# Kernel tuning notes

Hardware: AMD Instinct MI355X
Metric: run time of the kernel (lower is better)

The kernel has to match this reference:

```python
import jax, jax.numpy as jnp
import numpy as np

B, C, H, W = 16, 64, 64, 64
K = 1024  # n_embedding


def setup_inputs() -> dict:
    key = jax.random.key(0)
    k1, k2 = jax.random.split(key)
    x = jax.random.normal(k1, (B, C, H, W), dtype=jnp.float32)
    embedding = jax.random.normal(k2, (K, C), dtype=jnp.float32)
    return {"x": x, "embedding": embedding}


def reference(x, embedding):
    b, c, h, w = x.shape
    # [B,C,H,W] -> [N, C] tokens
    xf = jnp.transpose(x, (0, 2, 3, 1)).reshape(-1, c)
    # squared Euclidean distances (argmin-equivalent to torch.cdist p=2)
    d2 = (jnp.sum(xf * xf, axis=1, keepdims=True)
          - 2.0 * xf @ embedding.T
          + jnp.sum(embedding * embedding, axis=1)[None, :])  # [N, K]
    idx = jnp.argmin(d2, axis=-1)  # [N]
    q = embedding[idx]             # gather: [N, C]
    commitment_loss = jnp.mean((jax.lax.stop_gradient(q) - xf) ** 2)
    codebook_loss = jnp.mean((q - jax.lax.stop_gradient(xf)) ** 2)
    # straight-through estimator
    out = xf + jax.lax.stop_gradient(q - xf)
    x_q = jnp.transpose(out.reshape(b, h, w, c), (0, 3, 1, 2))
    indices = idx.reshape(-1, h, w)
    return x_q, codebook_loss, commitment_loss, indices
```

## Files before the change

kernel.cpp:

```cpp
#include <hip/hip_runtime.h>

typedef short s16x8 __attribute__((ext_vector_type(8)));
typedef float f32x4 __attribute__((ext_vector_type(4)));

#define NTOK 65536
#define CCH 64
#define KCB 1024
#define HWSZ 4096
#define CHW 262144
#define NXQ 4194304
#define NMEAN 4194304.0
#define PLANE_BYTES 131072

static __device__ __forceinline__ unsigned short f2bf(float f) {
    unsigned int u = __float_as_uint(f);
    return (unsigned short)((u + 0x7FFFu + ((u >> 16) & 1u)) >> 16);
}
static __device__ __forceinline__ float bf2f(unsigned short b) {
    return __uint_as_float(((unsigned int)b) << 16);
}

__global__ void vq_prep(const float* __restrict__ E, float* __restrict__ e2,
                        s16x8* __restrict__ Bh, s16x8* __restrict__ Bm,
                        s16x8* __restrict__ Bl, double* __restrict__ loss_acc) {
    int gid = blockIdx.x * blockDim.x + threadIdx.x;
    if (gid == 0) *loss_acc = 0.0;
    {
        int nt = gid >> 7, rem = gid & 127;
        int ks = rem >> 6, l = rem & 63;
        int code = nt * 16 + (l & 15);
        int cb   = ks * 32 + ((l >> 4) << 3);
        const float* ep = E + code * CCH + cb;
        s16x8 vh, vm, vl;
#pragma unroll
        for (int j = 0; j < 8; ++j) {
            float v = -2.f * ep[j];
            unsigned short h  = f2bf(v);  float r1 = v  - bf2f(h);
            unsigned short md = f2bf(r1); float r2 = r1 - bf2f(md);
            unsigned short lo = f2bf(r2);
            vh[j] = (short)h; vm[j] = (short)md; vl[j] = (short)lo;
        }
        Bh[gid] = vh; Bm[gid] = vm; Bl[gid] = vl;
    }
    if (gid < KCB) {
        const float4* e4 = reinterpret_cast<const float4*>(E + gid * CCH);
        float s = 0.f;
#pragma unroll
        for (int i = 0; i < 16; ++i) {
            float4 v = e4[i];
            s = fmaf(v.x, v.x, s); s = fmaf(v.y, v.y, s);
            s = fmaf(v.z, v.z, s); s = fmaf(v.w, v.w, s);
        }
        e2[gid] = s;
    }
}

__global__ __launch_bounds__(512, 2) void vq_main(
    const float* __restrict__ x, const float* __restrict__ E,
    const s16x8* __restrict__ Bh, const s16x8* __restrict__ Bm,
    const s16x8* __restrict__ Bl, const float* __restrict__ e2,
    float* __restrict__ out, double* __restrict__ loss_acc)
{
    __shared__ __align__(16) short XH[64 * 64];
    __shared__ __align__(16) short XM[64 * 64];
    __shared__ __align__(16) short XL[64 * 64];
    __shared__ float XSQ[8][64];
    __shared__ float SB[8][64];
    __shared__ int   SI[8][64];

    const int t    = threadIdx.x;
    const int lane = t & 63;
    const int w    = t >> 6;
    const int n0   = blockIdx.x * 64;
    const int b    = n0 >> 12;
    const int hw0  = n0 & 4095;

    {
        const int tok = t & 63;
        const int cb  = t >> 6;
        const float* xp = x + b * CHW + hw0 + tok;
        float xs = 0.f;
        s16x8 ph, pm, pl;
#pragma unroll
        for (int j = 0; j < 8; ++j) {
            float v = xp[(cb * 8 + j) * HWSZ];
            xs = fmaf(v, v, xs);
            unsigned short h  = f2bf(v);  float r1 = v  - bf2f(h);
            unsigned short md = f2bf(r1); float r2 = r1 - bf2f(md);
            unsigned short lo = f2bf(r2);
            ph[j] = (short)h; pm[j] = (short)md; pl[j] = (short)lo;
        }
        XSQ[cb][tok] = xs;
        const int wofs = tok * 128 + ((cb * 16) ^ ((tok & 7) << 4));
        *reinterpret_cast<s16x8*>((char*)XH + wofs) = ph;
        *reinterpret_cast<s16x8*>((char*)XM + wofs) = pm;
        *reinterpret_cast<s16x8*>((char*)XL + wofs) = pl;
    }
    __syncthreads();

    const int g   = lane >> 4;
    const int c15 = lane & 15;

    s16x8 ah[4][2], am[4][2], al[4][2];
#pragma unroll
    for (int m = 0; m < 4; ++m) {
        const int row = m * 16 + c15;
        const int rb  = row * 128;
        const int swz = (row & 7) << 4;
#pragma unroll
        for (int ks = 0; ks < 2; ++ks) {
            int off = rb + ((ks * 64 + g * 16) ^ swz);
            ah[m][ks] = *reinterpret_cast<const s16x8*>((const char*)XH + off);
            am[m][ks] = *reinterpret_cast<const s16x8*>((const char*)XM + off);
            al[m][ks] = *reinterpret_cast<const s16x8*>((const char*)XL + off);
        }
    }

    float e2w[8];
#pragma unroll
    for (int i = 0; i < 8; ++i) e2w[i] = e2[w * 128 + i * 16 + c15];

    float best[4][4];
    int   bidx[4][4];
#pragma unroll
    for (int m = 0; m < 4; ++m)
#pragma unroll
        for (int r = 0; r < 4; ++r) { best[m][r] = 3.4e38f; bidx[m][r] = 0; }

#pragma unroll 1
    for (int ch = 0; ch < 4; ++ch) {
        s16x8 bh[2][2], bm[2][2], bl[2][2];
#pragma unroll
        for (int nt = 0; nt < 2; ++nt)
#pragma unroll
            for (int ks = 0; ks < 2; ++ks) {
                int idx = ((w * 8 + ch * 2 + nt) * 2 + ks) * 64 + lane;
                bh[nt][ks] = Bh[idx];
                bm[nt][ks] = Bm[idx];
                bl[nt][ks] = Bl[idx];
            }

        f32x4 acc[4][2];
#pragma unroll
        for (int m = 0; m < 4; ++m)
#pragma unroll
            for (int nt = 0; nt < 2; ++nt) {
                float s0 = e2w[ch * 2 + nt];
                acc[m][nt] = (f32x4){s0, s0, s0, s0};
            }

#pragma unroll
        for (int m = 0; m < 4; ++m)
#pragma unroll
            for (int nt = 0; nt < 2; ++nt)
#pragma unroll
                for (int ks = 0; ks < 2; ++ks) {
                    acc[m][nt] = __builtin_amdgcn_mfma_f32_16x16x32_bf16(ah[m][ks], bh[nt][ks], acc[m][nt], 0, 0, 0);
                    acc[m][nt] = __builtin_amdgcn_mfma_f32_16x16x32_bf16(ah[m][ks], bm[nt][ks], acc[m][nt], 0, 0, 0);
                    acc[m][nt] = __builtin_amdgcn_mfma_f32_16x16x32_bf16(am[m][ks], bh[nt][ks], acc[m][nt], 0, 0, 0);
                    acc[m][nt] = __builtin_amdgcn_mfma_f32_16x16x32_bf16(am[m][ks], bm[nt][ks], acc[m][nt], 0, 0, 0);
                    acc[m][nt] = __builtin_amdgcn_mfma_f32_16x16x32_bf16(ah[m][ks], bl[nt][ks], acc[m][nt], 0, 0, 0);
                    acc[m][nt] = __builtin_amdgcn_mfma_f32_16x16x32_bf16(al[m][ks], bh[nt][ks], acc[m][nt], 0, 0, 0);
                }

#pragma unroll
        for (int nt = 0; nt < 2; ++nt) {
            const int k = w * 128 + ch * 32 + nt * 16 + c15;
#pragma unroll
            for (int m = 0; m < 4; ++m)
#pragma unroll
                for (int r = 0; r < 4; ++r) {
                    float s = acc[m][nt][r];
                    if (s < best[m][r]) { best[m][r] = s; bidx[m][r] = k; }
                }
        }
    }

#pragma unroll
    for (int m = 0; m < 4; ++m)
#pragma unroll
        for (int r = 0; r < 4; ++r) {
            float v = best[m][r]; int k = bidx[m][r];
#pragma unroll
            for (int off = 1; off < 16; off <<= 1) {
                float ov = __shfl_xor(v, off, 64);
                int   ok = __shfl_xor(k, off, 64);
                if (ov < v || (ov == v && ok < k)) { v = ov; k = ok; }
            }
            if (c15 == 0) {
                int tk = m * 16 + g * 4 + r;
                SB[w][tk] = v; SI[w][tk] = k;
            }
        }
    __syncthreads();

    if (w == 0) {
        float bv = SB[0][lane]; int bi = SI[0][lane];
#pragma unroll
        for (int ww = 1; ww < 8; ++ww) {
            float v = SB[ww][lane];
            if (v < bv) { bv = v; bi = SI[ww][lane]; }
        }
        out[NXQ + 2 + n0 + lane] = (float)bi;

        float xsq = 0.f;
#pragma unroll
        for (int c = 0; c < 8; ++c) xsq += XSQ[c][lane];
        float lsum = bv + xsq;
#pragma unroll
        for (int off = 32; off > 0; off >>= 1)
            lsum += __shfl_xor(lsum, off, 64);
        if (lane == 0) atomicAdd(loss_acc, (double)lsum);

        const float4* eq = reinterpret_cast<const float4*>(E + bi * CCH);
        float* oq = out + b * CHW + hw0 + lane;
#pragma unroll 1
        for (int gq = 0; gq < 4; ++gq) {
            float4 q0 = eq[4 * gq + 0];
            float4 q1 = eq[4 * gq + 1];
            float4 q2 = eq[4 * gq + 2];
            float4 q3 = eq[4 * gq + 3];
            float* o = oq + (16 * gq) * HWSZ;
            o[0 * HWSZ] = q0.x; o[1 * HWSZ]  = q0.y; o[2 * HWSZ]  = q0.z; o[3 * HWSZ]  = q0.w;
            o[4 * HWSZ] = q1.x; o[5 * HWSZ]  = q1.y; o[6 * HWSZ]  = q1.z; o[7 * HWSZ]  = q1.w;
            o[8 * HWSZ] = q2.x; o[9 * HWSZ]  = q2.y; o[10 * HWSZ] = q2.z; o[11 * HWSZ] = q2.w;
            o[12 * HWSZ] = q3.x; o[13 * HWSZ] = q3.y; o[14 * HWSZ] = q3.z; o[15 * HWSZ] = q3.w;
        }
    }
}

__global__ void vq_final(const double* __restrict__ loss_acc,
                         float* __restrict__ out) {
    if (threadIdx.x == 0) {
        float m = (float)(*loss_acc / NMEAN);
        out[NXQ]     = m;
        out[NXQ + 1] = m;
    }
}

extern "C" void kernel_launch(void* const* d_in, const int* in_sizes, int n_in,
                              void* d_out, int out_size, void* d_ws, size_t ws_size,
                              hipStream_t stream) {
    const float* x = (const float*)d_in[0];
    const float* E = (const float*)d_in[1];
    float* out = (float*)d_out;
    double* loss_acc = (double*)d_ws;
    float*  e2 = (float*)((char*)d_ws + 64);
    s16x8*  Bh = (s16x8*)((char*)d_ws + 8192);
    s16x8*  Bm = (s16x8*)((char*)d_ws + 8192 + PLANE_BYTES);
    s16x8*  Bl = (s16x8*)((char*)d_ws + 8192 + 2 * PLANE_BYTES);

    vq_prep <<<32,   256, 0, stream>>>(E, e2, Bh, Bm, Bl, loss_acc);
    vq_main <<<1024, 512, 0, stream>>>(x, E, Bh, Bm, Bl, e2, out, loss_acc);
    vq_final<<<1,    64,  0, stream>>>(loss_acc, out);
}
```

Before: 145.9 us.

## Restructure VQ kernel: warps own token tiles, stream codebook through double-buffered LDS

New measurement: 128.3 us. 12.0% less time.

```diff
diff --git a/kernel.cpp b/kernel.cpp
--- a/kernel.cpp
+++ b/kernel.cpp
@@ -3,7 +3,6 @@
 typedef short s16x8 __attribute__((ext_vector_type(8)));
 typedef float f32x4 __attribute__((ext_vector_type(4)));
 
-#define NTOK 65536
 #define CCH 64
 #define KCB 1024
 #define HWSZ 4096
@@ -55,132 +54,107 @@
     }
 }
 
-__global__ __launch_bounds__(512, 2) void vq_main(
+__global__ __launch_bounds__(256, 2) void vq_main(
     const float* __restrict__ x, const float* __restrict__ E,
     const s16x8* __restrict__ Bh, const s16x8* __restrict__ Bm,
     const s16x8* __restrict__ Bl, const float* __restrict__ e2,
     float* __restrict__ out, double* __restrict__ loss_acc)
 {
-    __shared__ __align__(16) short XH[64 * 64];
-    __shared__ __align__(16) short XM[64 * 64];
-    __shared__ __align__(16) short XL[64 * 64];
-    __shared__ float XSQ[8][64];
-    __shared__ float SB[8][64];
-    __shared__ int   SI[8][64];
+    __shared__ s16x8 BB[2][768];
+    __shared__ float BVL[128];
+    __shared__ int   BIL[128];
+    __shared__ float XSL[128];
 
     const int t    = threadIdx.x;
     const int lane = t & 63;
     const int w    = t >> 6;
-    const int n0   = blockIdx.x * 64;
+    const int g    = lane >> 4;
+    const int c15  = lane & 15;
+    const int n0   = blockIdx.x * 128;
     const int b    = n0 >> 12;
     const int hw0  = n0 & 4095;
 
-    {
-        const int tok = t & 63;
-        const int cb  = t >> 6;
-        const float* xp = x + b * CHW + hw0 + tok;
+    s16x8 ah[2][2], am[2][2], al[2][2];
+#pragma unroll
+    for (int mt = 0; mt < 2; ++mt) {
+        const float* xp = x + b * CHW + hw0 + w * 32 + mt * 16 + c15;
         float xs = 0.f;
-        s16x8 ph, pm, pl;
-#pragma unroll
-        for (int j = 0; j < 8; ++j) {
-            float v = xp[(cb * 8 + j) * HWSZ];
-            xs = fmaf(v, v, xs);
-            unsigned short h  = f2bf(v);  float r1 = v  - bf2f(h);
-            unsigned short md = f2bf(r1); float r2 = r1 - bf2f(md);
-            unsigned short lo = f2bf(r2);
-            ph[j] = (short)h; pm[j] = (short)md; pl[j] = (short)lo;
-        }
-        XSQ[cb][tok] = xs;
-        const int wofs = tok * 128 + ((cb * 16) ^ ((tok & 7) << 4));
-        *reinterpret_cast<s16x8*>((char*)XH + wofs) = ph;
-        *reinterpret_cast<s16x8*>((char*)XM + wofs) = pm;
-        *reinterpret_cast<s16x8*>((char*)XL + wofs) = pl;
-    }
+#pragma unroll
+        for (int ks = 0; ks < 2; ++ks)
+#pragma unroll
+            for (int j = 0; j < 8; ++j) {
+                float v = xp[(ks * 32 + g * 8 + j) * HWSZ];
+                xs = fmaf(v, v, xs);
+                unsigned short h  = f2bf(v);  float r1 = v  - bf2f(h);
+                unsigned short md = f2bf(r1); float r2 = r1 - bf2f(md);
+                unsigned short lo = f2bf(r2);
+                ah[mt][ks][j] = (short)h; am[mt][ks][j] = (short)md; al[mt][ks][j] = (short)lo;
+            }
+        xs += __shfl_xor(xs, 16, 64);
+        xs += __shfl_xor(xs, 32, 64);
+        if (lane < 16) XSL[w * 32 + mt * 16 + lane] = xs;
+    }
+
+    BB[0][t] = Bh[t]; BB[0][256 + t] = Bm[t]; BB[0][512 + t] = Bl[t];
     __syncthreads();
 
-    const int g   = lane >> 4;
-    const int c15 = lane & 15;
-
-    s16x8 ah[4][2], am[4][2], al[4][2];
-#pragma unroll
-    for (int m = 0; m < 4; ++m) {
-        const int row = m * 16 + c15;
-        const int rb  = row * 128;
-        const int swz = (row & 7) << 4;
-#pragma unroll
-        for (int ks = 0; ks < 2; ++ks) {
-            int off = rb + ((ks * 64 + g * 16) ^ swz);
-            ah[m][ks] = *reinterpret_cast<const s16x8*>((const char*)XH + off);
-            am[m][ks] = *reinterpret_cast<const s16x8*>((const char*)XM + off);
-            al[m][ks] = *reinterpret_cast<const s16x8*>((const char*)XL + off);
-        }
-    }
-
-    float e2w[8];
-#pragma unroll
-    for (int i = 0; i < 8; ++i) e2w[i] = e2[w * 128 + i * 16 + c15];
-
-    float best[4][4];
-    int   bidx[4][4];
-#pragma unroll
-    for (int m = 0; m < 4; ++m)
-#pragma unroll
-        for (int r = 0; r < 4; ++r) { best[m][r] = 3.4e38f; bidx[m][r] = 0; }
-
+    float best[2][4]; int bidx[2][4];
+#pragma unroll
+    for (int mt = 0; mt < 2; ++mt)
+#pragma unroll
+        for (int r = 0; r < 4; ++r) { best[mt][r] = 3.4e38f; bidx[mt][r] = 0; }
+
+    int buf = 0;
 #pragma unroll 1
-    for (int ch = 0; ch < 4; ++ch) {
-        s16x8 bh[2][2], bm[2][2], bl[2][2];
-#pragma unroll
-        for (int nt = 0; nt < 2; ++nt)
+    for (int ch = 0; ch < 32; ++ch) {
+        s16x8 sH, sM, sL;
+        const int nb = (ch + 1) * 256 + t;
+        if (ch < 31) { sH = Bh[nb]; sM = Bm[nb]; sL = Bl[nb]; }
+
+#pragma unroll
+        for (int nt = 0; nt < 2; ++nt) {
+            const float s0 = e2[ch * 32 + nt * 16 + c15];
+            s16x8 bh[2], bm[2], bl[2];
 #pragma unroll
             for (int ks = 0; ks < 2; ++ks) {
-                int idx = ((w * 8 + ch * 2 + nt) * 2 + ks) * 64 + lane;
-                bh[nt][ks] = Bh[idx];
-                bm[nt][ks] = Bm[idx];
-                bl[nt][ks] = Bl[idx];
-            }
-
-        f32x4 acc[4][2];
-#pragma unroll
-        for (int m = 0; m < 4; ++m)
-#pragma unroll
-            for (int nt = 0; nt < 2; ++nt) {
-                float s0 = e2w[ch * 2 + nt];
-                acc[m][nt] = (f32x4){s0, s0, s0, s0};
-            }
-
-#pragma unroll
-        for (int m = 0; m < 4; ++m)
-#pragma unroll
-            for (int nt = 0; nt < 2; ++nt)
+                const int q = (nt * 2 + ks) * 64 + lane;
+                bh[ks] = BB[buf][q];
+                bm[ks] = BB[buf][256 + q];
+                bl[ks] = BB[buf][512 + q];
+            }
+#pragma unroll
+            for (int mt = 0; mt < 2; ++mt) {
+                f32x4 acc = (f32x4){s0, s0, s0, s0};
 #pragma unroll
                 for (int ks = 0; ks < 2; ++ks) {
-                    acc[m][nt] = __builtin_amdgcn_mfma_f32_16x16x32_bf16(ah[m][ks], bh[nt][ks], acc[m][nt], 0, 0, 0);
-                    acc[m][nt] = __builtin_amdgcn_mfma_f32_16x16x32_bf16(ah[m][ks], bm[nt][ks], acc[m][nt], 0, 0, 0);
-                    acc[m][nt] = __builtin_amdgcn_mfma_f32_16x16x32_bf16(am[m][ks], bh[nt][ks], acc[m][nt], 0, 0, 0);
-                    acc[m][nt] = __builtin_amdgcn_mfma_f32_16x16x32_bf16(am[m][ks], bm[nt][ks], acc[m][nt], 0, 0, 0);
-                    acc[m][nt] = __builtin_amdgcn_mfma_f32_16x16x32_bf16(ah[m][ks], bl[nt][ks], acc[m][nt], 0, 0, 0);
-                    acc[m][nt] = __builtin_amdgcn_mfma_f32_16x16x32_bf16(al[m][ks], bh[nt][ks], acc[m][nt], 0, 0, 0);
+                    acc = __builtin_amdgcn_mfma_f32_16x16x32_bf16(ah[mt][ks], bh[ks], acc, 0, 0, 0);
+                    acc = __builtin_amdgcn_mfma_f32_16x16x32_bf16(ah[mt][ks], bm[ks], acc, 0, 0, 0);
+                    acc = __builtin_amdgcn_mfma_f32_16x16x32_bf16(am[mt][ks], bh[ks], acc, 0, 0, 0);
+                    acc = __builtin_amdgcn_mfma_f32_16x16x32_bf16(am[mt][ks], bm[ks], acc, 0, 0, 0);
+                    acc = __builtin_amdgcn_mfma_f32_16x16x32_bf16(ah[mt][ks], bl[ks], acc, 0, 0, 0);
+                    acc = __builtin_amdgcn_mfma_f32_16x16x32_bf16(al[mt][ks], bh[ks], acc, 0, 0, 0);
                 }
-
-#pragma unroll
-        for (int nt = 0; nt < 2; ++nt) {
-            const int k = w * 128 + ch * 32 + nt * 16 + c15;
-#pragma unroll
-            for (int m = 0; m < 4; ++m)
+                const int k = ch * 32 + nt * 16 + c15;
 #pragma unroll
                 for (int r = 0; r < 4; ++r) {
-                    float s = acc[m][nt][r];
-                    if (s < best[m][r]) { best[m][r] = s; bidx[m][r] = k; }
+                    float s = acc[r];
+                    if (s < best[mt][r]) { best[mt][r] = s; bidx[mt][r] = k; }
                 }
-        }
-    }
-
-#pragma unroll
-    for (int m = 0; m < 4; ++m)
+            }
+        }
+
+        if (ch < 31) {
+            BB[buf ^ 1][t] = sH; BB[buf ^ 1][256 + t] = sM; BB[buf ^ 1][512 + t] = sL;
+        }
+        __syncthreads();
+        buf ^= 1;
+    }
+
+#pragma unroll
+    for (int mt = 0; mt < 2; ++mt)
 #pragma unroll
         for (int r = 0; r < 4; ++r) {
-            float v = best[m][r]; int k = bidx[m][r];
+            float v = best[mt][r]; int k = bidx[mt][r];
 #pragma unroll
             for (int off = 1; off < 16; off <<= 1) {
                 float ov = __shfl_xor(v, off, 64);
@@ -188,43 +162,33 @@
                 if (ov < v || (ov == v && ok < k)) { v = ov; k = ok; }
             }
             if (c15 == 0) {
-                int tk = m * 16 + g * 4 + r;
-                SB[w][tk] = v; SI[w][tk] = k;
+                BVL[w * 32 + mt * 16 + g * 4 + r] = v;
+                BIL[w * 32 + mt * 16 + g * 4 + r] = k;
             }
         }
     __syncthreads();
 
-    if (w == 0) {
-        float bv = SB[0][lane]; int bi = SI[0][lane];
-#pragma unroll
-        for (int ww = 1; ww < 8; ++ww) {
-            float v = SB[ww][lane];
-            if (v < bv) { bv = v; bi = SI[ww][lane]; }
-        }
-        out[NXQ + 2 + n0 + lane] = (float)bi;
-
-        float xsq = 0.f;
-#pragma unroll
-        for (int c = 0; c < 8; ++c) xsq += XSQ[c][lane];
-        float lsum = bv + xsq;
-#pragma unroll
-        for (int off = 32; off > 0; off >>= 1)
-            lsum += __shfl_xor(lsum, off, 64);
-        if (lane == 0) atomicAdd(loss_acc, (double)lsum);
-
-        const float4* eq = reinterpret_cast<const float4*>(E + bi * CCH);
-        float* oq = out + b * CHW + hw0 + lane;
-#pragma unroll 1
-        for (int gq = 0; gq < 4; ++gq) {
-            float4 q0 = eq[4 * gq + 0];
-            float4 q1 = eq[4 * gq + 1];
-            float4 q2 = eq[4 * gq + 2];
-            float4 q3 = eq[4 * gq + 3];
-            float* o = oq + (16 * gq) * HWSZ;
-            o[0 * HWSZ] = q0.x; o[1 * HWSZ]  = q0.y; o[2 * HWSZ]  = q0.z; o[3 * HWSZ]  = q0.w;
-            o[4 * HWSZ] = q1.x; o[5 * HWSZ]  = q1.y; o[6 * HWSZ]  = q1.z; o[7 * HWSZ]  = q1.w;
-            o[8 * HWSZ] = q2.x; o[9 * HWSZ]  = q2.y; o[10 * HWSZ] = q2.z; o[11 * HWSZ] = q2.w;
-            o[12 * HWSZ] = q3.x; o[13 * HWSZ] = q3.y; o[14 * HWSZ] = q3.z; o[15 * HWSZ] = q3.w;
+    {
+        const int tok = (w & 1) * 64 + lane;
+        const int bi  = BIL[tok];
+        const int cq  = w >> 1;
+        const float4* eq = reinterpret_cast<const float4*>(E + bi * CCH + cq * 32);
+        float* oq = out + b * CHW + (cq * 32) * HWSZ + hw0 + tok;
+#pragma unroll
+        for (int i = 0; i < 8; ++i) {
+            float4 q = eq[i];
+            oq[(4 * i + 0) * HWSZ] = q.x;
+            oq[(4 * i + 1) * HWSZ] = q.y;
+            oq[(4 * i + 2) * HWSZ] = q.z;
+            oq[(4 * i + 3) * HWSZ] = q.w;
+        }
+        if (cq == 0) {
+            out[NXQ + 2 + n0 + tok] = (float)bi;
+            float lsum = BVL[tok] + XSL[tok];
+#pragma unroll
+            for (int off = 32; off > 0; off >>= 1)
+                lsum += __shfl_xor(lsum, off, 64);
+            if (lane == 0) atomicAdd(loss_acc, (double)lsum);
         }
     }
 }
@@ -250,7 +214,7 @@
     s16x8*  Bm = (s16x8*)((char*)d_ws + 8192 + PLANE_BYTES);
     s16x8*  Bl = (s16x8*)((char*)d_ws + 8192 + 2 * PLANE_BYTES);
 
-    vq_prep <<<32,   256, 0, stream>>>(E, e2, Bh, Bm, Bl, loss_acc);
-    vq_main <<<1024, 512, 0, stream>>>(x, E, Bh, Bm, Bl, e2, out, loss_acc);
-    vq_final<<<1,    64,  0, stream>>>(loss_acc, out);
-}
+    vq_prep <<<128, 64,  0, stream>>>(E, e2, Bh, Bm, Bl, loss_acc);
+    vq_main <<<512, 256, 0, stream>>>(x, E, Bh, Bm, Bl, e2, out, loss_acc);
+    vq_final<<<1,   64,  0, stream>>>(loss_acc, out);
+}
```
